# Kernel tuning notes

Hardware: AMD Instinct MI355X
Metric: run time of the kernel (lower is better)

Reference implementation:

```python
import jax, jax.numpy as jnp
import numpy as np

NUM_LABELS = 1000


def setup_inputs() -> dict:
    key = jax.random.key(0)
    k1, k2 = jax.random.split(key)
    outputs = jax.random.normal(k1, (64, 512, NUM_LABELS), dtype=jnp.float32)
    labels = jax.random.randint(k2, (64, 512), 0, NUM_LABELS, dtype=jnp.int32)
    return {"outputs": outputs, "labels": labels}


def reference(outputs, labels):
    L = outputs.shape[-1]
    flat = outputs.reshape(-1, L)        # [N, L]
    labs = labels.reshape(-1)            # [N]

    # State: index_selection [L] (the permutation torch derives via
    # argmax(encode_transfer, 1)) and unswitched-label membership mask [L].
    # torch.inner(ET, eye[select_col]) permutes ET's COLUMNS by select_col
    # (a transposition), which composes onto index_selection as
    # new_idx = select_col[old_idx].
    def step(carry, xs):
        idx_sel, unsw = carry
        y, lab = xs
        r = jnp.argmax(y[idx_sel]).astype(idx_sel.dtype)  # switched argmax
        lab_unsw = unsw[lab]
        do_swap = (r != lab) & lab_unsw
        # apply transposition (r <-> lab) to idx_sel when do_swap
        swapped = jnp.where(idx_sel == r, lab,
                            jnp.where(idx_sel == lab, r, idx_sel))
        new_idx = jnp.where(do_swap, swapped, idx_sel)
        # label is removed from unswitched set whenever it was a member
        # (both the mismatch-swap branch and the match branch remove it)
        new_unsw = unsw.at[lab].set(False)
        return (new_idx, new_unsw), None

    init = (jnp.arange(L, dtype=jnp.int32), jnp.ones((L,), dtype=bool))
    (idx_final, _), _ = jax.lax.scan(step, init, (flat, labs))

    # torch returns index_select on the flattened outputs with the FINAL
    # index_selection
    return jnp.take(flat, idx_final, axis=-1)
```

## Files before the change

kernel.cpp:

```cpp
#include <hip/hip_runtime.h>
#include <climits>
#include <cstdint>

#define L 1000
#define NROWS 32768


__global__ void k_init(int* __restrict__ first_row, int* __restrict__ evt_slot) {
    int i = blockIdx.x * blockDim.x + threadIdx.x;
    if (i < NROWS) evt_slot[i] = -1;
    if (i < L) first_row[i] = INT_MAX;
}

__global__ void k_first(const int* __restrict__ labels, int* __restrict__ first_row) {
    int i = blockIdx.x * blockDim.x + threadIdx.x;
    if (i < NROWS) atomicMin(&first_row[labels[i]], i);
}

__global__ void k_argmax(const float* __restrict__ flat, const int* __restrict__ first_row,
                         int* __restrict__ evt_slot) {
    int lab = blockIdx.x;
    int row = first_row[lab];
    if (row == INT_MAX) return;
    const float* y = flat + (size_t)row * L;
    int tid = threadIdx.x;
    float bv = -INFINITY;
    int bk = 0x7fffffff;
    for (int k = tid; k < L; k += 256) {
        float v = y[k];
        if (v > bv) { bv = v; bk = k; }
    }
    __shared__ float sv[256];
    __shared__ int   sk[256];
    sv[tid] = bv; sk[tid] = bk;
    __syncthreads();
    for (int off = 128; off > 0; off >>= 1) {
        if (tid < off) {
            float v2 = sv[tid + off]; int k2 = sk[tid + off];
            if (v2 > sv[tid] || (v2 == sv[tid] && k2 < sk[tid])) { sv[tid] = v2; sk[tid] = k2; }
        }
        __syncthreads();
    }
    if (tid == 0) evt_slot[row] = (lab << 10) | sk[0];
}

__global__ void __launch_bounds__(1024) k_seq(const int* __restrict__ evt_slot,
                                              int* __restrict__ perm_g) {
    __shared__ int evt[1025];
    __shared__ int pos[L];
    __shared__ int scnt[1024];
    int tid = threadIdx.x;
    int base = tid * 32;
    int c = 0;
    for (int j = 0; j < 32; j++) c += (evt_slot[base + j] >= 0) ? 1 : 0;
    scnt[tid] = c;
    __syncthreads();
    for (int off = 1; off < 1024; off <<= 1) {
        int v = scnt[tid];
        int add = (tid >= off) ? scnt[tid - off] : 0;
        __syncthreads();
        scnt[tid] = v + add;
        __syncthreads();
    }
    int K = scnt[1023];
    int w = tid ? scnt[tid - 1] : 0;
    for (int j = 0; j < 32; j++) {
        int v = evt_slot[base + j];
        if (v >= 0) evt[w++] = v;
    }
    if (tid < L) pos[tid] = tid;
    __syncthreads();
    if (tid == 0 && K > 0) {
        evt[K] = evt[K - 1];
        int v0 = evt[0];
        int lab = v0 >> 10, m = v0 & 1023;
        int Pm = pos[m], Plab = pos[lab];
        for (int i = 0; i < K; i++) {
            int vn   = evt[i + 1];
            int labn = vn >> 10, mn = vn & 1023;
            int Pmn   = pos[mn];
            int Plabn = pos[labn];
            int r = Pm;
            if (r != lab) {
                int pr = pos[r];
                pos[r]   = Plab;
                pos[lab] = pr;
                if (mn == r)        Pmn = Plab;
                else if (mn == lab) Pmn = pr;
                if (labn == r)        Plabn = Plab;
                else if (labn == lab) Plabn = pr;
            }
            Pm = Pmn; Plab = Plabn; lab = labn; m = mn;
        }
    }
    __syncthreads();
    if (tid < L) perm_g[pos[tid]] = tid;
}

__global__ void __launch_bounds__(1024) k_gather(const float* __restrict__ flat,
                                                 const int* __restrict__ perm_g,
                                                 float* __restrict__ out) {
    __shared__ __align__(16) int   p[1024];
    __shared__ __align__(16) float buf[4][L];
    int tid = threadIdx.x;
    if (tid < L) p[tid] = perm_g[tid];
    int g = tid >> 8;
    int t = tid & 255;
    size_t row = (size_t)blockIdx.x * 4 + g;
    const float* src = flat + row * L;
    float*       dst = out  + row * L;
    float4 v;
    if (t < 250) v = ((const float4*)src)[t];
    __syncthreads();
    if (t < 250) ((float4*)buf[g])[t] = v;
    __syncthreads();
    if (t < 250) {
        int j = t * 4;
        float4 o;
        o.x = buf[g][p[j + 0]];
        o.y = buf[g][p[j + 1]];
        o.z = buf[g][p[j + 2]];
        o.w = buf[g][p[j + 3]];
        ((float4*)dst)[t] = o;
    }
}

extern "C" void kernel_launch(void* const* d_in, const int* in_sizes, int n_in,
                              void* d_out, int out_size, void* d_ws, size_t ws_size,
                              hipStream_t stream) {
    const float* flat   = (const float*)d_in[0];
    const int*   labels = (const int*)d_in[1];
    float* out = (float*)d_out;
    int* ws = (int*)d_ws;
    int* first_row = ws;
    int* perm_g    = ws + 1024;
    int* evt_slot  = ws + 2048;

    k_init  <<<(NROWS + 255) / 256, 256, 0, stream>>>(first_row, evt_slot);
    k_first <<<(NROWS + 255) / 256, 256, 0, stream>>>(labels, first_row);
    k_argmax<<<L, 256, 0, stream>>>(flat, first_row, evt_slot);
    k_seq   <<<1, 1024, 0, stream>>>(evt_slot, perm_g);
    k_gather<<<NROWS / 4, 1024, 0, stream>>>(flat, perm_g, out);
}
```

Baseline: 347.4 us.

## Compact events by rank in argmax kernel and pipeline serial swap loop two ahead

Each argmax block now counts how many labels have an earlier first row and writes its event directly to that compacted slot. This removes the 32K-entry event sentinel init and the block-wide prefix scan over all rows in the sequential kernel. The single-thread swap loop now prefetches position lookups two events ahead so shared-memory loads overlap the dependent chain. The cost is extra bookkeeping for forwarding pending swaps into both lookahead slots, plus an extra 1000-entry count read per argmax block.

```diff
diff --git a/kernel.cpp b/kernel.cpp
--- a/kernel.cpp
+++ b/kernel.cpp
@@ -6,9 +6,8 @@
 #define NROWS 32768
 
 
-__global__ void k_init(int* __restrict__ first_row, int* __restrict__ evt_slot) {
+__global__ void k_init(int* __restrict__ first_row) {
     int i = blockIdx.x * blockDim.x + threadIdx.x;
-    if (i < NROWS) evt_slot[i] = -1;
     if (i < L) first_row[i] = INT_MAX;
 }
 
@@ -18,10 +17,10 @@
 }
 
 __global__ void k_argmax(const float* __restrict__ flat, const int* __restrict__ first_row,
-                         int* __restrict__ evt_slot) {
+                         int* __restrict__ evt_g) {
     int lab = blockIdx.x;
     int row = first_row[lab];
-    if (row == INT_MAX) return;
+    if (row >= NROWS) return;
     const float* y = flat + (size_t)row * L;
     int tid = threadIdx.x;
     float bv = -INFINITY;
@@ -30,67 +29,64 @@
         float v = y[k];
         if (v > bv) { bv = v; bk = k; }
     }
+    int cnt = 0;
+    for (int j = tid; j < L; j += 256) cnt += (first_row[j] < row) ? 1 : 0;
     __shared__ float sv[256];
     __shared__ int   sk[256];
-    sv[tid] = bv; sk[tid] = bk;
+    __shared__ int   sc[256];
+    sv[tid] = bv; sk[tid] = bk; sc[tid] = cnt;
     __syncthreads();
     for (int off = 128; off > 0; off >>= 1) {
         if (tid < off) {
             float v2 = sv[tid + off]; int k2 = sk[tid + off];
             if (v2 > sv[tid] || (v2 == sv[tid] && k2 < sk[tid])) { sv[tid] = v2; sk[tid] = k2; }
+            sc[tid] += sc[tid + off];
         }
         __syncthreads();
     }
-    if (tid == 0) evt_slot[row] = (lab << 10) | sk[0];
+    if (tid == 0) evt_g[sc[0]] = (lab << 10) | sk[0];
 }
 
-__global__ void __launch_bounds__(1024) k_seq(const int* __restrict__ evt_slot,
+__global__ void __launch_bounds__(1024) k_seq(const int* __restrict__ first_row,
+                                              const int* __restrict__ evt_g,
                                               int* __restrict__ perm_g) {
-    __shared__ int evt[1025];
+    __shared__ int evt[1008];
     __shared__ int pos[L];
-    __shared__ int scnt[1024];
     int tid = threadIdx.x;
-    int base = tid * 32;
-    int c = 0;
-    for (int j = 0; j < 32; j++) c += (evt_slot[base + j] >= 0) ? 1 : 0;
-    scnt[tid] = c;
-    __syncthreads();
-    for (int off = 1; off < 1024; off <<= 1) {
-        int v = scnt[tid];
-        int add = (tid >= off) ? scnt[tid - off] : 0;
-        __syncthreads();
-        scnt[tid] = v + add;
-        __syncthreads();
-    }
-    int K = scnt[1023];
-    int w = tid ? scnt[tid - 1] : 0;
-    for (int j = 0; j < 32; j++) {
-        int v = evt_slot[base + j];
-        if (v >= 0) evt[w++] = v;
-    }
+    int present = (tid < L) && (first_row[tid] < NROWS);
+    int K = __syncthreads_count(present);
+    if (tid < K) evt[tid] = evt_g[tid];
+    if (tid >= K && tid < K + 4) evt[tid] = 0;
     if (tid < L) pos[tid] = tid;
     __syncthreads();
     if (tid == 0 && K > 0) {
-        evt[K] = evt[K - 1];
-        int v0 = evt[0];
-        int lab = v0 >> 10, m = v0 & 1023;
-        int Pm = pos[m], Plab = pos[lab];
+        int e0 = evt[0], e1 = evt[1], e2 = evt[2];
+        int m   = e0 & 1023, lab = e0 >> 10;
+        int Pm  = m,  Plab = lab;
+        int m1  = e1 & 1023, l1  = e1 >> 10;
+        int Pm1 = m1, Pl1 = l1;
         for (int i = 0; i < K; i++) {
-            int vn   = evt[i + 1];
-            int labn = vn >> 10, mn = vn & 1023;
-            int Pmn   = pos[mn];
-            int Plabn = pos[labn];
-            int r = Pm;
+            int r  = Pm;
+            int pr = pos[r];
+            int m2 = e2 & 1023, l2 = e2 >> 10;
+            int nPm = pos[m2];
+            int nPl = pos[l2];
+            int e3  = evt[i + 3];
             if (r != lab) {
-                int pr = pos[r];
                 pos[r]   = Plab;
                 pos[lab] = pr;
-                if (mn == r)        Pmn = Plab;
-                else if (mn == lab) Pmn = pr;
-                if (labn == r)        Plabn = Plab;
-                else if (labn == lab) Plabn = pr;
+                if      (m1 == r)   Pm1 = Plab;
+                else if (m1 == lab) Pm1 = pr;
+                if      (l1 == r)   Pl1 = Plab;
+                else if (l1 == lab) Pl1 = pr;
+                if      (m2 == r)   nPm = Plab;
+                else if (m2 == lab) nPm = pr;
+                if      (l2 == r)   nPl = Plab;
+                else if (l2 == lab) nPl = pr;
             }
-            Pm = Pmn; Plab = Plabn; lab = labn; m = mn;
+            m  = m1; lab = l1; Pm  = Pm1; Plab = Pl1;
+            m1 = m2; l1  = l2; Pm1 = nPm; Pl1  = nPl;
+            e2 = e3;
         }
     }
     __syncthreads();
@@ -133,12 +129,12 @@
     float* out = (float*)d_out;
     int* ws = (int*)d_ws;
     int* first_row = ws;
-    int* perm_g    = ws + 1024;
-    int* evt_slot  = ws + 2048;
+    int* evt_g     = ws + 1024;
+    int* perm_g    = ws + 2048;
 
-    k_init  <<<(NROWS + 255) / 256, 256, 0, stream>>>(first_row, evt_slot);
+    k_init  <<<(L + 255) / 256, 256, 0, stream>>>(first_row);
     k_first <<<(NROWS + 255) / 256, 256, 0, stream>>>(labels, first_row);
-    k_argmax<<<L, 256, 0, stream>>>(flat, first_row, evt_slot);
-    k_seq   <<<1, 1024, 0, stream>>>(evt_slot, perm_g);
+    k_argmax<<<L, 256, 0, stream>>>(flat, first_row, evt_g);
+    k_seq   <<<1, 1024, 0, stream>>>(first_row, evt_g, perm_g);
     k_gather<<<NROWS / 4, 1024, 0, stream>>>(flat, perm_g, out);
 }
```

Result: slower. 376.0 us (+8.2%).
